# Performance work log

Hardware: AMD Instinct MI355X
Metric: run time of the kernel (lower is better)

Reference implementation:

```python
import jax, jax.numpy as jnp
import numpy as np

QMAX8 = 127.0  # 2**(8-1)-1


def quant1(x, scale):
    # 1-bit symmetric quant: s * sign(x), s = |scale| (per-group mean scale)
    return jnp.abs(scale) * jnp.sign(x)


def quant8(x, scale):
    s = jnp.maximum(jnp.abs(scale), 1e-8)
    q = jnp.clip(jnp.round(x / s), -QMAX8, QMAX8)
    return q * s


def setup_inputs() -> dict:
    key = jax.random.key(0)
    ks = jax.random.split(key, 5)
    p, j, k, m, l, n = 2, 32, 32, 32, 8, 32
    x = jax.random.normal(ks[0], (2, 1024, k * n), dtype=jnp.float32)
    Y_fp = jax.random.normal(ks[1], (p, j, k, m, l), dtype=jnp.float32)
    Z_fp = jax.random.normal(ks[2], (p, j, k, l, n), dtype=jnp.float32)
    A = jax.random.normal(ks[3], (p, j, k, 4), dtype=jnp.float32)
    bias = jax.random.normal(ks[4], (j * m,), dtype=jnp.float32)
    act_scale = jnp.full((1,), 0.001, dtype=jnp.float32)
    return {"x": x, "Y_fp": Y_fp, "Z_fp": Z_fp, "A": A, "bias": bias,
            "act_scale": act_scale}


def reference(x, Y_fp, Z_fp, A, bias, act_scale):
    p, j, k, m, l = Y_fp.shape
    n = Z_fp.shape[-1]
    orig_shape = x.shape[:-1]
    X = x.astype(jnp.float32)
    X = quant8(X, act_scale)  # activation quantization (act_bits=8)

    # per-(p,j,k) mean-abs scales over last two dims
    Y_scale = jnp.mean(jnp.abs(Y_fp), axis=(-2, -1), keepdims=True)
    Z_scale = jnp.mean(jnp.abs(Z_fp), axis=(-2, -1), keepdims=True)
    Y_q = quant1(Y_fp, Y_scale)  # (p,j,k,m,l)
    Z_q = quant1(Z_fp, Z_scale)  # (p,j,k,l,n)

    X_kn = X.reshape(-1, k, n)  # (B,k,n)
    T = jnp.einsum('bkn,pjkln->bpjkl', X_kn, Z_q)
    core = jnp.einsum('pjkml,bpjkl->bpjkm', Y_q, T)

    # quant_bias=True correction terms
    a = A[..., 0][None, ..., None]            # (1,p,j,k,1)
    out1 = jnp.sum(core * a, axis=(1, 3))     # (B,j,m)
    Y_sum = jnp.sum(Y_q, axis=-1)             # (p,j,k,m)
    B_coef = jnp.sum(A[..., 1][..., None] * Y_sum, axis=0)  # (j,k,m)
    Sx = jnp.sum(X_kn, axis=-1)               # (B,k)
    out2 = jnp.einsum('bk,jkm->bjm', Sx, B_coef)
    Zs = jnp.sum(Z_q, axis=-2)                # (p,j,k,n)
    Tz = jnp.einsum('bkn,pjkn->bpjk', X_kn, Zs)
    out3 = jnp.sum(Tz * A[..., 2][None], axis=(1, 3))[..., None]  # (B,j,1)
    D_coef = jnp.sum(A[..., 3], axis=0)       # (j,k)
    out4 = jnp.einsum('bk,jk->bj', Sx, D_coef)[..., None]          # (B,j,1)

    out_bjm = out1 + out2 + out3 + out4       # (B,j,m) via broadcast
    out_2d = out_bjm.reshape(-1, j * m) + bias
    out = out_2d.reshape(*orig_shape, j * m)
    return out.astype(x.dtype)
```

## Files before the change

### kernel.cpp

```cpp
#include <hip/hip_runtime.h>
#include <math.h>
#include <stdint.h>


typedef __attribute__((ext_vector_type(8))) short bf16x8;
typedef __attribute__((ext_vector_type(4))) float f32x4;
typedef __attribute__((ext_vector_type(4))) unsigned short us4;

__device__ __forceinline__ float fsign(float v) {
    return (v > 0.f) ? 1.f : ((v < 0.f) ? -1.f : 0.f);
}

__device__ __forceinline__ unsigned short f2bf(float f) {
    union { float f; uint32_t u; } c; c.f = f;
    uint32_t r = 0x7fffu + ((c.u >> 16) & 1u);
    return (unsigned short)((c.u + r) >> 16);
}

__device__ __forceinline__ void gl2lds16(const void* g, void* l) {
    __builtin_amdgcn_global_load_lds(
        (const __attribute__((address_space(1))) void*)g,
        (__attribute__((address_space(3))) void*)l, 16, 0, 0);
}

__global__ __launch_bounds__(256) void fused_pre(
    const float* __restrict__ Y,
    const float* __restrict__ Z,
    const float* __restrict__ A,
    const float* __restrict__ x,
    const float* __restrict__ act_scale,
    unsigned short* __restrict__ wt,
    unsigned short* __restrict__ qx)
{
    const int t = threadIdx.x;

    if (blockIdx.x >= 1024) {
        const float s = fmaxf(fabsf(act_scale[0]), 1e-8f);
        const int b2 = blockIdx.x - 1024;
        #pragma unroll
        for (int it = 0; it < 4; ++it) {
            const size_t i4 = (size_t)b2 * 256 + t + (size_t)it * 131072;
            const float4 v = *(const float4*)(x + i4 * 4);
            us4 o;
            o.x = f2bf(fminf(fmaxf(rintf(v.x / s), -127.f), 127.f));
            o.y = f2bf(fminf(fmaxf(rintf(v.y / s), -127.f), 127.f));
            o.z = f2bf(fminf(fmaxf(rintf(v.z / s), -127.f), 127.f));
            o.w = f2bf(fminf(fmaxf(rintf(v.w / s), -127.f), 127.f));
            *(us4*)(qx + i4 * 4) = o;
        }
        return;
    }

    __shared__ float sgy[256];
    __shared__ float sgz[256];
    __shared__ float wred[8];

    const int jk = blockIdx.x;
    const int jj = jk >> 5;
    const int kk = jk & 31;
    const int n  = t & 31;
    const int mb = t >> 5;

    float acc[4] = {0.f, 0.f, 0.f, 0.f};

    for (int p = 0; p < 2; ++p) {
        const int base = ((p * 32 + jj) * 32 + kk);
        const float yv = Y[(size_t)base * 256 + t];
        const float zv = Z[(size_t)base * 256 + t];
        sgy[t] = fsign(yv);
        sgz[t] = fsign(zv);

        float ay = fabsf(yv), az = fabsf(zv);
        #pragma unroll
        for (int d = 1; d < 64; d <<= 1) {
            ay += __shfl_xor(ay, d, 64);
            az += __shfl_xor(az, d, 64);
        }
        if ((t & 63) == 0) {
            wred[(t >> 6) * 2 + 0] = ay;
            wred[(t >> 6) * 2 + 1] = az;
        }
        __syncthreads();

        const float sY = (wred[0] + wred[2] + wred[4] + wred[6]) * (1.f / 256.f);
        const float sZ = (wred[1] + wred[3] + wred[5] + wred[7]) * (1.f / 256.f);
        const float a0 = A[(size_t)base * 4 + 0];
        const float a1 = A[(size_t)base * 4 + 1];
        const float a2 = A[(size_t)base * 4 + 2];
        const float a3 = A[(size_t)base * 4 + 3];

        float zcol = 0.f;
        #pragma unroll
        for (int l = 0; l < 8; ++l) zcol += sgz[l * 32 + n];

        #pragma unroll
        for (int q = 0; q < 4; ++q) {
            const int m = mb + 8 * q;
            float ysum = 0.f, w = 0.f;
            #pragma unroll
            for (int l = 0; l < 8; ++l) {
                const float ys = sgy[m * 8 + l];
                ysum += ys;
                w += ys * sgz[l * 32 + n];
            }
            acc[q] += a0 * sY * sZ * w + a1 * sY * ysum + a2 * sZ * zcol + a3;
        }
        __syncthreads();
    }

    #pragma unroll
    for (int q = 0; q < 4; ++q) {
        const int m = mb + 8 * q;
        wt[(size_t)(jj * 32 + m) * 1024 + kk * 32 + n] = f2bf(acc[q]);
    }
}

__global__ __launch_bounds__(256) void gemm_mfma(
    const unsigned short* __restrict__ qx,
    const unsigned short* __restrict__ wt,
    const float* __restrict__ bias,
    const float* __restrict__ act_scale,
    float* __restrict__ out)
{
    __shared__ __align__(16) short lds[2 * 6144];

    const int tid  = threadIdx.x;
    const int lane = tid & 63;
    const int wave = tid >> 6;
    const int wm = wave >> 1;
    const int wn = wave & 1;
    const int rowBase = blockIdx.y * 64;
    const int colBase = blockIdx.x * 128;

    const float s = fmaxf(fabsf(act_scale[0]), 1e-8f);

    f32x4 acc[2][4];
    #pragma unroll
    for (int i = 0; i < 2; ++i)
        #pragma unroll
        for (int jx = 0; jx < 4; ++jx)
            acc[i][jx] = (f32x4)0.f;

    const unsigned short* agp =
        qx + (size_t)(rowBase + (tid >> 2)) * 1024 + (tid & 3) * 8;
    const unsigned short* bgp0 =
        wt + (size_t)(colBase + (tid >> 2)) * 1024 + (tid & 3) * 8;
    const unsigned short* bgp1 = bgp0 + (size_t)64 * 1024;

    char* const ldsc = (char*)lds;
    const int q4  = lane >> 4;
    const int l16 = lane & 15;

    {
        char* b = ldsc;
        gl2lds16(agp,  b + wave * 1024);
        gl2lds16(bgp0, b + 4096 + wave * 1024);
        gl2lds16(bgp1, b + 8192 + wave * 1024);
    }

    for (int kt = 0; kt < 32; ++kt) {
        __syncthreads();
        const int cur = kt & 1;

        if (kt + 1 < 32) {
            const int k1 = (kt + 1) * 32;
            char* b = ldsc + (cur ^ 1) * 12288;
            gl2lds16(agp  + k1, b + wave * 1024);
            gl2lds16(bgp0 + k1, b + 4096 + wave * 1024);
            gl2lds16(bgp1 + k1, b + 8192 + wave * 1024);
        }

        const short* As = lds + cur * 6144;
        const short* Bs = As + 2048;

        bf16x8 af[2], bfr[4];
        #pragma unroll
        for (int im = 0; im < 2; ++im)
            af[im] = *(const bf16x8*)&As[(wm * 32 + im * 16 + l16) * 32 + q4 * 8];
        #pragma unroll
        for (int in = 0; in < 4; ++in)
            bfr[in] = *(const bf16x8*)&Bs[(wn * 64 + in * 16 + l16) * 32 + q4 * 8];

        #pragma unroll
        for (int im = 0; im < 2; ++im)
            #pragma unroll
            for (int in = 0; in < 4; ++in)
                acc[im][in] = __builtin_amdgcn_mfma_f32_16x16x32_bf16(
                    af[im], bfr[in], acc[im][in], 0, 0, 0);
    }

    #pragma unroll
    for (int im = 0; im < 2; ++im) {
        #pragma unroll
        for (int in = 0; in < 4; ++in) {
            const int col = colBase + wn * 64 + in * 16 + l16;
            const float b = bias[col];
            #pragma unroll
            for (int r = 0; r < 4; ++r) {
                const int row = rowBase + wm * 32 + im * 16 + q4 * 4 + r;
                out[(size_t)row * 1024 + col] = s * acc[im][in][r] + b;
            }
        }
    }
}

extern "C" void kernel_launch(void* const* d_in, const int* in_sizes, int n_in,
                              void* d_out, int out_size, void* d_ws, size_t ws_size,
                              hipStream_t stream) {
    const float* x         = (const float*)d_in[0];
    const float* Y_fp      = (const float*)d_in[1];
    const float* Z_fp      = (const float*)d_in[2];
    const float* A         = (const float*)d_in[3];
    const float* bias      = (const float*)d_in[4];
    const float* act_scale = (const float*)d_in[5];
    float* out = (float*)d_out;

    unsigned short* wt = (unsigned short*)d_ws;
    unsigned short* qx = (unsigned short*)((char*)d_ws + 2 * 1024 * 1024);

    fused_pre<<<dim3(1536), dim3(256), 0, stream>>>(Y_fp, Z_fp, A, x, act_scale, wt, qx);
    gemm_mfma<<<dim3(8, 32), dim3(256), 0, stream>>>(qx, wt, bias, act_scale, out);
}
```

Baseline: 87.49 us.

## Triple-buffer GEMM LDS loads with explicit vmcnt waits; merge p-loop in preprocessing

The GEMM moves from a double-buffered to a triple-buffered LDS pipeline. It prefetches three K-tiles and uses explicit s_waitcnt vmcnt counts plus raw barriers, so loads run further ahead of the MFMA work. The weight-preprocessing kernel now handles both p slices at once instead of looping, which cuts barriers and lets the loads overlap. The cost is more LDS per block, which may lower occupancy, and hand-written waitcnt logic that depends on exact load counts.

```diff
diff --git a/kernel.cpp b/kernel.cpp
--- a/kernel.cpp
+++ b/kernel.cpp
@@ -51,9 +51,9 @@
         return;
     }
 
-    __shared__ float sgy[256];
-    __shared__ float sgz[256];
-    __shared__ float wred[8];
+    __shared__ float sgy[2][256];
+    __shared__ float sgz[2][256];
+    __shared__ float wred[16];
 
     const int jk = blockIdx.x;
     const int jj = jk >> 5;
@@ -61,57 +61,70 @@
     const int n  = t & 31;
     const int mb = t >> 5;
 
-    float acc[4] = {0.f, 0.f, 0.f, 0.f};
-
-    for (int p = 0; p < 2; ++p) {
-        const int base = ((p * 32 + jj) * 32 + kk);
-        const float yv = Y[(size_t)base * 256 + t];
-        const float zv = Z[(size_t)base * 256 + t];
-        sgy[t] = fsign(yv);
-        sgz[t] = fsign(zv);
-
-        float ay = fabsf(yv), az = fabsf(zv);
-        #pragma unroll
-        for (int d = 1; d < 64; d <<= 1) {
-            ay += __shfl_xor(ay, d, 64);
-            az += __shfl_xor(az, d, 64);
-        }
-        if ((t & 63) == 0) {
-            wred[(t >> 6) * 2 + 0] = ay;
-            wred[(t >> 6) * 2 + 1] = az;
-        }
-        __syncthreads();
-
-        const float sY = (wred[0] + wred[2] + wred[4] + wred[6]) * (1.f / 256.f);
-        const float sZ = (wred[1] + wred[3] + wred[5] + wred[7]) * (1.f / 256.f);
-        const float a0 = A[(size_t)base * 4 + 0];
-        const float a1 = A[(size_t)base * 4 + 1];
-        const float a2 = A[(size_t)base * 4 + 2];
-        const float a3 = A[(size_t)base * 4 + 3];
-
-        float zcol = 0.f;
-        #pragma unroll
-        for (int l = 0; l < 8; ++l) zcol += sgz[l * 32 + n];
-
-        #pragma unroll
-        for (int q = 0; q < 4; ++q) {
-            const int m = mb + 8 * q;
-            float ysum = 0.f, w = 0.f;
-            #pragma unroll
-            for (int l = 0; l < 8; ++l) {
-                const float ys = sgy[m * 8 + l];
-                ysum += ys;
-                w += ys * sgz[l * 32 + n];
-            }
-            acc[q] += a0 * sY * sZ * w + a1 * sY * ysum + a2 * sZ * zcol + a3;
-        }
-        __syncthreads();
+    const int base0 = jj * 32 + kk;
+    const int base1 = 1024 + base0;
+
+    const float yv0 = Y[(size_t)base0 * 256 + t];
+    const float yv1 = Y[(size_t)base1 * 256 + t];
+    const float zv0 = Z[(size_t)base0 * 256 + t];
+    const float zv1 = Z[(size_t)base1 * 256 + t];
+    const float a00 = A[(size_t)base0 * 4 + 0], a01 = A[(size_t)base0 * 4 + 1];
+    const float a02 = A[(size_t)base0 * 4 + 2], a03 = A[(size_t)base0 * 4 + 3];
+    const float a10 = A[(size_t)base1 * 4 + 0], a11 = A[(size_t)base1 * 4 + 1];
+    const float a12 = A[(size_t)base1 * 4 + 2], a13 = A[(size_t)base1 * 4 + 3];
+
+    sgy[0][t] = fsign(yv0);
+    sgy[1][t] = fsign(yv1);
+    sgz[0][t] = fsign(zv0);
+    sgz[1][t] = fsign(zv1);
+
+    float ay0 = fabsf(yv0), az0 = fabsf(zv0);
+    float ay1 = fabsf(yv1), az1 = fabsf(zv1);
+    #pragma unroll
+    for (int d = 1; d < 64; d <<= 1) {
+        ay0 += __shfl_xor(ay0, d, 64);
+        az0 += __shfl_xor(az0, d, 64);
+        ay1 += __shfl_xor(ay1, d, 64);
+        az1 += __shfl_xor(az1, d, 64);
+    }
+    if ((t & 63) == 0) {
+        const int w = t >> 6;
+        wred[w * 4 + 0] = ay0;
+        wred[w * 4 + 1] = az0;
+        wred[w * 4 + 2] = ay1;
+        wred[w * 4 + 3] = az1;
+    }
+    __syncthreads();
+
+    const float sY0 = (wred[0] + wred[4] + wred[8]  + wred[12]) * (1.f / 256.f);
+    const float sZ0 = (wred[1] + wred[5] + wred[9]  + wred[13]) * (1.f / 256.f);
+    const float sY1 = (wred[2] + wred[6] + wred[10] + wred[14]) * (1.f / 256.f);
+    const float sZ1 = (wred[3] + wred[7] + wred[11] + wred[15]) * (1.f / 256.f);
+
+    float zcol0 = 0.f, zcol1 = 0.f;
+    #pragma unroll
+    for (int l = 0; l < 8; ++l) {
+        zcol0 += sgz[0][l * 32 + n];
+        zcol1 += sgz[1][l * 32 + n];
     }
 
     #pragma unroll
     for (int q = 0; q < 4; ++q) {
         const int m = mb + 8 * q;
-        wt[(size_t)(jj * 32 + m) * 1024 + kk * 32 + n] = f2bf(acc[q]);
+        float ysum0 = 0.f, w0 = 0.f, ysum1 = 0.f, w1 = 0.f;
+        #pragma unroll
+        for (int l = 0; l < 8; ++l) {
+            const float ys0 = sgy[0][m * 8 + l];
+            const float ys1 = sgy[1][m * 8 + l];
+            ysum0 += ys0;
+            ysum1 += ys1;
+            w0 += ys0 * sgz[0][l * 32 + n];
+            w1 += ys1 * sgz[1][l * 32 + n];
+        }
+        const float acc =
+            a00 * sY0 * sZ0 * w0 + a01 * sY0 * ysum0 + a02 * sZ0 * zcol0 + a03 +
+            a10 * sY1 * sZ1 * w1 + a11 * sY1 * ysum1 + a12 * sZ1 * zcol1 + a13;
+        wt[(size_t)(jj * 32 + m) * 1024 + kk * 32 + n] = f2bf(acc);
     }
 }
 
@@ -122,7 +135,7 @@
     const float* __restrict__ act_scale,
     float* __restrict__ out)
 {
-    __shared__ __align__(16) short lds[2 * 6144];
+    __shared__ __align__(16) short lds[3 * 6144];
 
     const int tid  = threadIdx.x;
     const int lane = tid & 63;
@@ -150,26 +163,24 @@
     char* const ldsc = (char*)lds;
     const int q4  = lane >> 4;
     const int l16 = lane & 15;
-
-    {
-        char* b = ldsc;
-        gl2lds16(agp,  b + wave * 1024);
-        gl2lds16(bgp0, b + 4096 + wave * 1024);
-        gl2lds16(bgp1, b + 8192 + wave * 1024);
-    }
-
+    const int woff = wave * 1024;
+
+    #pragma unroll
+    for (int tpre = 0; tpre < 3; ++tpre) {
+        char* b = ldsc + tpre * 12288;
+        gl2lds16(agp  + tpre * 32, b + woff);
+        gl2lds16(bgp0 + tpre * 32, b + 4096 + woff);
+        gl2lds16(bgp1 + tpre * 32, b + 8192 + woff);
+    }
+
+    #pragma unroll 1
     for (int kt = 0; kt < 32; ++kt) {
-        __syncthreads();
-        const int cur = kt & 1;
-
-        if (kt + 1 < 32) {
-            const int k1 = (kt + 1) * 32;
-            char* b = ldsc + (cur ^ 1) * 12288;
-            gl2lds16(agp  + k1, b + wave * 1024);
-            gl2lds16(bgp0 + k1, b + 4096 + wave * 1024);
-            gl2lds16(bgp1 + k1, b + 8192 + wave * 1024);
-        }
-
+        if (kt < 30)       asm volatile("s_waitcnt vmcnt(6)" ::: "memory");
+        else if (kt == 30) asm volatile("s_waitcnt vmcnt(3)" ::: "memory");
+        else               asm volatile("s_waitcnt vmcnt(0)" ::: "memory");
+        __builtin_amdgcn_s_barrier();
+
+        const int cur = kt % 3;
         const short* As = lds + cur * 6144;
         const short* Bs = As + 2048;
 
@@ -180,6 +191,17 @@
         #pragma unroll
         for (int in = 0; in < 4; ++in)
             bfr[in] = *(const bf16x8*)&Bs[(wn * 64 + in * 16 + l16) * 32 + q4 * 8];
+
+        asm volatile("s_waitcnt lgkmcnt(0)" ::: "memory");
+        __builtin_amdgcn_s_barrier();
+
+        if (kt + 3 < 32) {
+            const int k3 = (kt + 3) * 32;
+            char* b = ldsc + cur * 12288;
+            gl2lds16(agp  + k3, b + woff);
+            gl2lds16(bgp0 + k3, b + 4096 + woff);
+            gl2lds16(bgp1 + k3, b + 8192 + woff);
+        }
 
         #pragma unroll
         for (int im = 0; im < 2; ++im)
```

Measured after the change: 86.95 us. No clear change (-0.6%).
